# Kernel tuning notes

Hardware: AMD Instinct MI355X
Metric: run time of the kernel (lower is better)

## Reference

```python
import jax, jax.numpy as jnp
import numpy as np
import math

H = 1024      # d_input / d_output channels
N = 64        # d_state (diagonal SSM size)
L = 2048      # kernel / sequence length
DT_MIN, DT_MAX = 0.001, 0.1
HIGH_STAB, LOW_STAB = -0.9, -0.8


def setup_inputs() -> dict:
    key = jax.random.key(0)
    k1, k2, k3, k4 = jax.random.split(key, 4)
    # log_dt ~ U[log(dt_min), log(dt_max)]
    log_dt = jax.random.uniform(k1, (H,), dtype=jnp.float32) \
        * (math.log(DT_MAX) - math.log(DT_MIN)) + math.log(DT_MIN)
    # C ~ complex normal, stored as real pairs (H, N, 2) like torch.view_as_real
    C = jax.random.normal(k2, (H, N, 2), dtype=jnp.float32)
    # Diagonal A: Re(A) uniform in [high_stability, low_stability] (stable),
    # Im(A) random; stored as real pairs (N, 2). A is a frozen buffer.
    a_re = jax.random.uniform(k3, (N,), dtype=jnp.float32) * (LOW_STAB - HIGH_STAB) + HIGH_STAB
    a_im = jax.random.normal(k4, (N,), dtype=jnp.float32) * math.pi
    A = jnp.stack([a_re, a_im], axis=-1)
    return {"log_dt": log_dt, "C": C, "A": A, "input_length": L}


def reference(log_dt, C, A, input_length):
    # log_dt: (H,) float32; C: (H,N,2) float32; A: (N,2) float32
    dt = jnp.exp(log_dt)                                   # (H,)
    Cc = (C[..., 0] + 1j * C[..., 1]).astype(jnp.complex64)  # (H, N)
    Ac = (A[..., 0] + 1j * A[..., 1]).astype(jnp.complex64)  # (N,)
    dtA = dt[:, None].astype(jnp.complex64) * Ac[None, :]  # (H, N)
    # Vandermonde-style kernel: exp(dtA * l) for l in [0, L)
    l = jnp.arange(input_length, dtype=jnp.float32).astype(jnp.complex64)  # (L,)
    Kexp = jnp.exp(dtA[:, :, None] * l[None, None, :])     # (H, N, L) complex64
    Cmod = Cc * (jnp.exp(dtA) - 1.0) / Ac                  # (H, N)
    K = 2.0 * jnp.einsum('hn,hnl->hl', Cmod, Kexp).real    # (H, L) float32
    return K
```

## Files before the change

kernel.cpp:

```cpp
#include <hip/hip_runtime.h>

#define H 1024
#define N 64
#define L 2048
#define TPB 256
#define KK 4
#define NBLK (H * 2)

#define INV2PI 0.15915494309189535f

typedef float f32x2 __attribute__((ext_vector_type(2)));

__device__ __forceinline__ f32x2 cmul(f32x2 w, f32x2 s) {
    f32x2 t, r;
    asm("v_pk_mul_f32 %0, %1, %2 op_sel_hi:[1,0]"
        : "=v"(t) : "v"(w), "v"(s));
    asm("v_pk_fma_f32 %0, %1, %2, %3 op_sel:[1,1,0] op_sel_hi:[0,1,1] neg_lo:[1,0,0]"
        : "=v"(r) : "v"(w), "v"(s), "v"(t));
    return r;
}

__device__ __forceinline__ f32x2 cexp_rev(float mag_arg, float rev_arg) {
    float m = __expf(mag_arg);
    float rv = rev_arg - floorf(rev_arg);
    f32x2 e;
    e.x = m * __builtin_amdgcn_cosf(rv);
    e.y = m * __builtin_amdgcn_sinf(rv);
    return e;
}

__global__ __launch_bounds__(TPB, 8) void s4d_fused(const float* __restrict__ log_dt,
                                                    const float* __restrict__ Cv,
                                                    const float* __restrict__ Av,
                                                    float* __restrict__ out)
{
    __shared__ f32x2 W16[N][16];
    __shared__ f32x2 E1t[N][16];
    __shared__ f32x2 Sv[N];

    const int b    = blockIdx.x;
    const int h    = b >> 1;
    const int half = b & 1;
    const int t    = threadIdx.x;

    {
        const int n  = t >> 2;
        const int j0 = (t & 3) << 2;
        float dt = __expf(log_dt[h]);

        float2 a2 = ((const float2*)Av)[n];
        float dr    = dt * a2.x;
        float direv = dt * a2.y * INV2PI;

        f32x2 r1 = cexp_rev(dr, direv);
        float2 c2 = ((const float2*)Cv)[h * N + n];
        float er = r1.x - 1.0f, ei = r1.y;
        float tr = c2.x * er - c2.y * ei;
        float ti = c2.x * ei + c2.y * er;
        float inv = 2.0f / (a2.x * a2.x + a2.y * a2.y);
        f32x2 cm;
        cm.x = (tr * a2.x + ti * a2.y) * inv;
        cm.y = (ti * a2.x - tr * a2.y) * inv;

        const float off = (float)(half << 10);
#pragma unroll
        for (int jj = 0; jj < 4; ++jj) {
            float fj = (float)(j0 + jj);
            E1t[n][j0 + jj] = cexp_rev(dr * fj, direv * fj);
            float fg = fj * 16.0f + off;
            W16[n][j0 + jj] = cmul(cexp_rev(dr * fg, direv * fg), cm);
        }

        if (t < N) {
            float2 a2b = ((const float2*)Av)[t];
            float drb = dt * a2b.x;
            float dib = dt * a2b.y * INV2PI;
            Sv[t] = cexp_rev(drb * 256.0f, dib * 256.0f);
        }
    }
    __syncthreads();

    float acc[KK];
#pragma unroll
    for (int k = 0; k < KK; ++k) acc[k] = 0.0f;

    const int jhi = t >> 4;
    const int jlo = t & 15;

#pragma unroll 2
    for (int n = 0; n < N; ++n) {
        f32x2 w16 = W16[n][jhi];
        f32x2 e1  = E1t[n][jlo];
        f32x2 s   = Sv[n];
        f32x2 w = cmul(e1, w16);

#pragma unroll
        for (int k = 0; k < KK; ++k) {
            acc[k] += w.x;
            w = cmul(w, s);
        }
    }

    float* o = out + h * L + (half << 10) + t;
#pragma unroll
    for (int k = 0; k < KK; ++k) o[k * TPB] = acc[k];
}

extern "C" void kernel_launch(void* const* d_in, const int* in_sizes, int n_in,
                              void* d_out, int out_size, void* d_ws, size_t ws_size,
                              hipStream_t stream) {
    const float* log_dt = (const float*)d_in[0];
    const float* Cv     = (const float*)d_in[1];
    const float* Av     = (const float*)d_in[2];
    float* out          = (float*)d_out;

    s4d_fused<<<NBLK, TPB, 0, stream>>>(log_dt, Cv, Av, out);
}
```

Before: 76.38 us.

## Split state dimension across waves and use real second-order recurrence

```diff
diff --git a/kernel.cpp b/kernel.cpp
--- a/kernel.cpp
+++ b/kernel.cpp
@@ -4,8 +4,10 @@
 #define N 64
 #define L 2048
 #define TPB 256
-#define KK 4
+#define HALF_L 1024
 #define NBLK (H * 2)
+#define KPT 16
+#define NPW 16
 
 #define INV2PI 0.15915494309189535f
 
@@ -34,9 +36,10 @@
                                                     const float* __restrict__ Av,
                                                     float* __restrict__ out)
 {
-    __shared__ f32x2 W16[N][16];
-    __shared__ f32x2 E1t[N][16];
-    __shared__ f32x2 Sv[N];
+    __shared__ __align__(16) char smem[16384];
+    float4* CF = (float4*)smem;
+    f32x2*  W4 = (f32x2*)(smem + 1024);
+    f32x2*  E1 = (f32x2*)(smem + 3072);
 
     const int b    = blockIdx.x;
     const int h    = b >> 1;
@@ -44,8 +47,8 @@
     const int t    = threadIdx.x;
 
     {
-        const int n  = t >> 2;
-        const int j0 = (t & 3) << 2;
+        const int n = t >> 2;
+        const int q = t & 3;
         float dt = __expf(log_dt[h]);
 
         float2 a2 = ((const float2*)Av)[n];
@@ -62,48 +65,63 @@
         cm.x = (tr * a2.x + ti * a2.y) * inv;
         cm.y = (ti * a2.x - tr * a2.y) * inv;
 
-        const float off = (float)(half << 10);
 #pragma unroll
         for (int jj = 0; jj < 4; ++jj) {
-            float fj = (float)(j0 + jj);
-            E1t[n][j0 + jj] = cexp_rev(dr * fj, direv * fj);
-            float fg = fj * 16.0f + off;
-            W16[n][j0 + jj] = cmul(cexp_rev(dr * fg, direv * fg), cm);
+            float fj = (float)(q * 4 + jj);
+            E1[n * 16 + q * 4 + jj] = cexp_rev(dr * fj, direv * fj);
         }
-
-        if (t < N) {
-            float2 a2b = ((const float2*)Av)[t];
-            float drb = dt * a2b.x;
-            float dib = dt * a2b.y * INV2PI;
-            Sv[t] = cexp_rev(drb * 256.0f, dib * 256.0f);
+        float fg = 16.0f * (float)q + 1024.0f * (float)half;
+        W4[n * 4 + q] = cmul(cexp_rev(dr * fg, direv * fg), cm);
+        if (q == 0) {
+            f32x2 s = cexp_rev(dr * 64.0f, direv * 64.0f);
+            CF[n] = make_float4(s.x, s.y, 2.0f * s.x, -(s.x * s.x + s.y * s.y));
         }
     }
     __syncthreads();
 
-    float acc[KK];
+    const int w   = t >> 6;
+    const int j   = t & 63;
+    const int jhi = j >> 4;
+    const int jlo = j & 15;
+    const int n0  = w * NPW;
+
+    float acc[KPT];
 #pragma unroll
-    for (int k = 0; k < KK; ++k) acc[k] = 0.0f;
-
-    const int jhi = t >> 4;
-    const int jlo = t & 15;
+    for (int k = 0; k < KPT; ++k) acc[k] = 0.0f;
 
 #pragma unroll 2
-    for (int n = 0; n < N; ++n) {
-        f32x2 w16 = W16[n][jhi];
-        f32x2 e1  = E1t[n][jlo];
-        f32x2 s   = Sv[n];
-        f32x2 w = cmul(e1, w16);
+    for (int ni = 0; ni < NPW; ++ni) {
+        const int n = n0 + ni;
+        f32x2 w4  = W4[n * 4 + jhi];
+        f32x2 e1  = E1[n * 16 + jlo];
+        float4 cf = CF[n];
 
+        f32x2 w0 = cmul(e1, w4);
+        float u0 = w0.x, v0 = w0.y;
+        float u1 = u0 * cf.x - v0 * cf.y;
+        acc[0] += u0;
+        acc[1] += u1;
 #pragma unroll
-        for (int k = 0; k < KK; ++k) {
-            acc[k] += w.x;
-            w = cmul(w, s);
+        for (int k = 2; k < KPT; ++k) {
+            float u2 = cf.z * u1 + cf.w * u0;
+            acc[k] += u2;
+            u0 = u1; u1 = u2;
         }
     }
+    __syncthreads();
 
-    float* o = out + h * L + (half << 10) + t;
+    float* part = (float*)smem;
 #pragma unroll
-    for (int k = 0; k < KK; ++k) o[k * TPB] = acc[k];
+    for (int k = 0; k < KPT; ++k)
+        part[w * HALF_L + j + 64 * k] = acc[k];
+    __syncthreads();
+
+    float* o = out + h * L + (half << 10);
+#pragma unroll
+    for (int k2 = 0; k2 < 4; ++k2) {
+        int l = t + 256 * k2;
+        o[l] = part[l] + part[HALF_L + l] + part[2 * HALF_L + l] + part[3 * HALF_L + l];
+    }
 }
 
 extern "C" void kernel_launch(void* const* d_in, const int* in_sizes, int n_in,
```

After: 77.69 us. No clear change (+1.7%).
